# Kernel optimization log

Hardware: AMD Instinct MI355X
Metric: run time of the kernel (lower is better)

Reference implementation:

```python
import jax, jax.numpy as jnp
import numpy as np

B, T = 2, 2048
DENSE = 1024
SPARSE = 1024
NH = 8
HD = SPARSE // NH          # 128
WINDOW = 64
K = 32
RANK = HD // 4             # 32
GATE_THRESH = 0.2


def setup_inputs() -> dict:
    key = jax.random.key(0)
    ks = jax.random.split(key, 12)
    return {
        "x": jax.random.normal(ks[0], (B, T, DENSE), dtype=jnp.float32),
        "enc_q": jax.random.normal(ks[1], (NH, DENSE, HD), dtype=jnp.float32) * 0.02,
        "enc_v": jax.random.normal(ks[2], (NH, DENSE, HD), dtype=jnp.float32) * 0.02,
        # metric network: Linear(SPARSE, SPARSE//2) -> GELU -> Linear(SPARSE//2, NH*HD)
        "metric_w1": jax.random.normal(ks[3], (SPARSE, SPARSE // 2), dtype=jnp.float32) * (1.0 / np.sqrt(SPARSE)),
        "metric_b1": jnp.zeros((SPARSE // 2,), dtype=jnp.float32),
        "metric_w2": jax.random.normal(ks[4], (SPARSE // 2, NH * HD), dtype=jnp.float32) * (1.0 / np.sqrt(SPARSE // 2)),
        "metric_b2": jnp.zeros((NH * HD,), dtype=jnp.float32),
        "base_metric": jnp.ones((NH, HD), dtype=jnp.float32) * 0.1,
        "hebb_U": jax.random.normal(ks[5], (NH, HD, RANK), dtype=jnp.float32) * 0.01,
        "hebb_V": jax.random.normal(ks[6], (NH, RANK, HD), dtype=jnp.float32) * 0.01,
        "decoder": jax.random.normal(ks[7], (NH * HD, DENSE), dtype=jnp.float32) * 0.02,
    }


def _causal_window_indices(t_len, window):
    pos = jnp.arange(t_len)
    off = jnp.arange(window)
    idx = jnp.clip(pos[:, None] - off[None, :], 0, t_len - 1)  # (T, W)
    mask = idx <= pos[:, None]
    return idx, mask


def _dynamic_metric(field, w1, b1, w2, b2, base):
    # field: (B, T, SPARSE)
    sig = field.mean(axis=1)
    if field.shape[1] >= 8:
        sig = sig + field[:, ::8].mean(axis=1) * 0.5
    h = jax.nn.gelu(sig @ w1 + b1, approximate=False)
    mod = (h @ w2 + b2).reshape(field.shape[0], NH, HD)
    return jax.nn.softplus(base[None] + 0.1 * mod)  # (B, NH, HD)


def reference(x, enc_q, enc_v, metric_w1, metric_b1, metric_w2, metric_b2,
              base_metric, hebb_U, hebb_V, decoder):
    Bb, Tt, _ = x.shape
    query_sparse = jax.nn.relu(jnp.einsum('btd,nde->btne', x, enc_q))  # (B,T,NH,HD)
    value_sparse = jax.nn.relu(jnp.einsum('btd,nde->btne', x, enc_v))

    metric = _dynamic_metric(query_sparse.reshape(Bb, Tt, NH * HD),
                             metric_w1, metric_b1, metric_w2, metric_b2, base_metric)

    idx, mask = _causal_window_indices(Tt, WINDOW)  # (T,W)
    idx_b = jnp.broadcast_to(idx[None], (Bb, Tt, WINDOW))
    batch_ix = jnp.arange(Bb)[:, None, None]

    outs = []
    for h in range(NH):
        q_h = query_sparse[:, :, h, :]   # (B,T,HD)
        v_h = value_sparse[:, :, h, :]
        m_h = metric[:, h][:, None, None, :]  # (B,1,1,HD)

        k_windows = q_h[:, idx, :]            # (B,T,W,HD) gather
        diff = k_windows - q_h[:, :, None, :]
        dist = jnp.sqrt((diff * diff * m_h).sum(axis=-1) + 1e-8)  # (B,T,W)
        dist = jnp.where(mask[None], dist, jnp.inf)

        neg_d, loc = jax.lax.top_k(-dist, K)  # smallest-K distances
        topd = -neg_d
        top_idx = jnp.take_along_axis(idx_b, loc, axis=2)  # (B,T,K)

        infl = jnp.exp(-topd)
        infl = infl / (infl.sum(axis=-1, keepdims=True) + 1e-8)

        neighbor_v = v_h[batch_ix, top_idx]   # (B,T,K,HD)
        context = jnp.einsum('btk,btkd->btd', infl, neighbor_v)

        q_norm = jnp.linalg.norm(q_h, axis=-1, keepdims=True)
        gate = (q_norm > GATE_THRESH).astype(q_h.dtype)
        heb_mat = hebb_U[h] @ hebb_V[h]       # (HD,HD)
        q_unit = q_h / jnp.maximum(q_norm, 1e-12)  # F.normalize
        heb_ctx = q_unit @ heb_mat
        context = context + gate * 0.1 * heb_ctx

        outs.append(q_h * context)

    out_sparse = jnp.stack(outs, axis=2)           # (B,T,NH,HD)
    return out_sparse.reshape(Bb, Tt, NH * HD) @ decoder
```

## Files before the change

kernel.cpp:

```cpp
#include <hip/hip_runtime.h>
#include <math.h>

#define T_ 2048
#define NH_ 8
#define HD_ 128

typedef unsigned short u16;
typedef short bf16x8 __attribute__((ext_vector_type(8)));
typedef _Float16 f16x8 __attribute__((ext_vector_type(8)));
typedef float f32x4 __attribute__((ext_vector_type(4)));

union FH { _Float16 h; u16 u; };

__device__ __forceinline__ u16 f2h(float f)
{
    FH c; c.h = (_Float16)f; return c.u;
}
__device__ __forceinline__ float h2f(u16 v)
{
    FH c; c.u = v; return (float)c.h;
}
__device__ __forceinline__ void split1h(float f, u16& h, u16& l)
{
    h = f2h(f);
    l = f2h(f - h2f(h));
}

__device__ __forceinline__ u16 f2bf(float f)
{
    unsigned u = __float_as_uint(f);
    return (u16)((u + 0x7FFFu + ((u >> 16) & 1u)) >> 16);
}
__device__ __forceinline__ float bf2f(u16 h)
{
    return __uint_as_float(((unsigned)h) << 16);
}


__global__ __launch_bounds__(256) void cvt_in(const float* __restrict__ x,
                                              const float* __restrict__ enc_q,
                                              const float* __restrict__ enc_v,
                                              u16* __restrict__ xh,
                                              u16* __restrict__ WTh)
{
    __shared__ u16 tH[32][33];
    const int bid = blockIdx.x;
    if (bid < 4096) {
        int i = (bid * 256 + threadIdx.x) * 4;
        int m = i >> 10, k = i & 1023;
        float4 v = *(const float4*)&x[i];
        ushort4 hv = {f2h(v.x), f2h(v.y), f2h(v.z), f2h(v.w)};
        long o = (long)(m >> 6) * 65536 + (k >> 5) * 2048
               + ((k >> 3) & 3) * 512 + (m & 63) * 8 + (k & 7);
        *(ushort4*)&xh[o] = hv;
    } else {
        int rb = bid - 4096;
        int bx = rb & 31, by = (rb >> 5) & 31, bz = rb >> 10;
        const float* Bw = bz ? enc_v : enc_q;
        const int nofs = bz << 10;
        const int tid = threadIdx.x;
        const int tx = tid & 31, ty = tid >> 5;
        const int k0 = bx * 32, c0 = by * 32;
        #pragma unroll
        for (int r = 0; r < 4; ++r) {
            int k = k0 + ty * 4 + r;
            int c = c0 + tx;
            float v = Bw[(long)(c >> 7) * 131072 + (long)k * 128 + (c & 127)];
            tH[ty * 4 + r][tx] = f2h(v);
        }
        __syncthreads();
        #pragma unroll
        for (int r = 0; r < 4; ++r) {
            int n = nofs + c0 + ty * 4 + r;
            int k = k0 + tx;
            long o = (long)(n >> 6) * 65536 + (k >> 5) * 2048
                   + ((k >> 3) & 3) * 512 + (n & 63) * 8 + (k & 7);
            WTh[o] = tH[tx][ty * 4 + r];
        }
    }
}

__global__ __launch_bounds__(256) void cvt_wT_pk(const float* __restrict__ src0,
                                                 u16* __restrict__ WTh,
                                                 int Kd, int cs, int cm, long sn, int sk)
{
    __shared__ u16 tH[32][33];
    const float* Bw = src0;
    const int tid = threadIdx.x;
    const int tx = tid & 31, ty = tid >> 5;
    const int k0 = blockIdx.x * 32, c0 = blockIdx.y * 32;
    #pragma unroll
    for (int r = 0; r < 4; ++r) {
        int k = k0 + ty * 4 + r;
        int c = c0 + tx;
        float v = Bw[(long)(c >> cs) * sn + (long)k * sk + (c & cm)];
        tH[ty * 4 + r][tx] = f2h(v);
    }
    __syncthreads();
    const long sstr = (long)Kd * 64;
    #pragma unroll
    for (int r = 0; r < 4; ++r) {
        int n = c0 + ty * 4 + r;
        int k = k0 + tx;
        long o = (long)(n >> 6) * sstr + (k >> 5) * 2048
               + ((k >> 3) & 3) * 512 + (n & 63) * 8 + (k & 7);
        WTh[o] = tH[tx][ty * 4 + r];
    }
}

__global__ __launch_bounds__(256, 1) void gemm_qv(
    const u16* __restrict__ Ah, const u16* __restrict__ Bh,
    float* __restrict__ Qf, u16* __restrict__ Vh,
    float* __restrict__ Ps, float* __restrict__ Ps8, int Kd)
{
    __shared__ __align__(16) u16 S[4][6144];

    const int tid  = threadIdx.x;
    const int w    = tid >> 6;
    const int lane = tid & 63;

    const int id   = blockIdx.x;
    const int m0   = (id & 31) * 128;
    const int n0   = (id >> 5) * 256;

    const int mw   = (w & 1) * 64, nw = (w >> 1) * 128;
    const int mr   = lane & 15, quad = lane >> 4;

    const long sstr = (long)Kd * 64;
    const u16* gAh = Ah + (long)((m0 + mw) >> 6) * sstr;
    const u16* gB0 = Bh + (long)((n0 + nw) >> 6) * sstr;
    const u16* gB1 = gB0 + sstr;

    u16* W = &S[w][0];

    f32x4 acc[4][8] = {};
    uint4 a0, a1, a2, a3;
    uint4 b0, b1, b2, b3, b4, b5, b6, b7;

#define LOADG(KT) do { long t = (long)(KT) * 2048 + lane * 8;                        \
    a0 = *(const uint4*)(gAh + t +    0); a1 = *(const uint4*)(gAh + t +  512);      \
    a2 = *(const uint4*)(gAh + t + 1024); a3 = *(const uint4*)(gAh + t + 1536);      \
    b0 = *(const uint4*)(gB0 + t +    0); b1 = *(const uint4*)(gB0 + t +  512);      \
    b2 = *(const uint4*)(gB0 + t + 1024); b3 = *(const uint4*)(gB0 + t + 1536);      \
    b4 = *(const uint4*)(gB1 + t +    0); b5 = *(const uint4*)(gB1 + t +  512);      \
    b6 = *(const uint4*)(gB1 + t + 1024); b7 = *(const uint4*)(gB1 + t + 1536); } while (0)

#define STOREG() do { u16* D = W + lane * 8;                                         \
    *(uint4*)(D +    0) = a0; *(uint4*)(D +  512) = a1;                              \
    *(uint4*)(D + 1024) = a2; *(uint4*)(D + 1536) = a3;                              \
    *(uint4*)(D + 2048) = b0; *(uint4*)(D + 2560) = b1;                              \
    *(uint4*)(D + 3072) = b2; *(uint4*)(D + 3584) = b3;                              \
    *(uint4*)(D + 4096) = b4; *(uint4*)(D + 4608) = b5;                              \
    *(uint4*)(D + 5120) = b6; *(uint4*)(D + 5632) = b7; } while (0)

    LOADG(0);
    STOREG();
    LOADG(1);

    const int NT = Kd >> 5;
    for (int kt = 0; kt < NT; ++kt) {
        f16x8 fah[4], fbh[8];
        #pragma unroll
        for (int i = 0; i < 4; ++i)
            fah[i] = *(const f16x8*)(W + quad * 512 + (i * 16 + mr) * 8);
        #pragma unroll
        for (int j = 0; j < 8; ++j)
            fbh[j] = *(const f16x8*)(W + 2048 + ((j < 4) ? 0 : 2048)
                                     + quad * 512 + ((j & 3) * 16 + mr) * 8);
        if (kt + 1 < NT) STOREG();
        if (kt + 2 < NT) LOADG(kt + 2);
        #pragma unroll
        for (int i = 0; i < 4; ++i)
            #pragma unroll
            for (int j = 0; j < 8; ++j)
                acc[i][j] = __builtin_amdgcn_mfma_f32_16x16x32_f16(fah[i], fbh[j], acc[i][j], 0, 0, 0);
    }
#undef LOADG
#undef STOREG

    if (n0 < 1024) {
        #pragma unroll
        for (int i = 0; i < 4; ++i)
            #pragma unroll
            for (int j = 0; j < 8; ++j)
                #pragma unroll
                for (int r = 0; r < 4; ++r) {
                    float v = fmaxf(acc[i][j][r], 0.f);
                    acc[i][j][r] = v;
                    int row = m0 + mw + i * 16 + quad * 4 + r;
                    int col = n0 + nw + j * 16 + mr;
                    Qf[(long)row * 1024 + col] = v;
                }
        int slot = (id & 31) * 2 + (w & 1);
        #pragma unroll
        for (int j = 0; j < 8; ++j) {
            float ps = 0.f, p8 = 0.f;
            #pragma unroll
            for (int i = 0; i < 4; ++i) {
                #pragma unroll
                for (int r = 0; r < 4; ++r) ps += acc[i][j][r];
                if ((quad & 1) == 0) p8 += acc[i][j][0];
            }
            ps += __shfl_xor(ps, 16, 64); ps += __shfl_xor(ps, 32, 64);
            p8 += __shfl_xor(p8, 16, 64); p8 += __shfl_xor(p8, 32, 64);
            if (quad == 0) {
                int col = n0 + nw + j * 16 + mr;
                Ps [slot * 1024 + col] = ps;
                Ps8[slot * 1024 + col] = p8;
            }
        }
    } else {
        #pragma unroll
        for (int i = 0; i < 4; ++i)
            #pragma unroll
            for (int j = 0; j < 8; ++j)
                #pragma unroll
                for (int r = 0; r < 4; ++r) {
                    float v = fmaxf(acc[i][j][r], 0.f);
                    int row = m0 + mw + i * 16 + quad * 4 + r;
                    int col = n0 - 1024 + nw + j * 16 + mr;
                    Vh[(long)row * 1024 + col] = f2h(v);
                }
    }
}

__global__ __launch_bounds__(256, 1) void gemm_dec(
    const u16* __restrict__ Ah, const u16* __restrict__ Bh,
    float* __restrict__ C, int N, int Kd)
{
    __shared__ __align__(16) u16 S[4][4096];

    const int tid  = threadIdx.x;
    const int w    = tid >> 6;
    const int lane = tid & 63;

    const int id   = blockIdx.x;
    const int m0   = (((id & 7) << 2) + ((id >> 3) & 3)) * 128;
    const int n0   = (id >> 5) * 128;

    const int mw   = (w & 1) * 64, nw = (w >> 1) * 64;
    const int mr   = lane & 15, quad = lane >> 4;

    const long sstr = (long)Kd * 64;
    const u16* gAh = Ah + (long)((m0 + mw) >> 6) * sstr;
    const u16* gBh = Bh + (long)((n0 + nw) >> 6) * sstr;

    u16* W = &S[w][0];

    f32x4 acc[4][4] = {};
    uint4 a0, a1, a2, a3, b0, b1, b2, b3;

#define LOADG(KT) do { long t = (long)(KT) * 2048 + lane * 8;                        \
    a0 = *(const uint4*)(gAh + t +    0); a1 = *(const uint4*)(gAh + t +  512);      \
    a2 = *(const uint4*)(gAh + t + 1024); a3 = *(const uint4*)(gAh + t + 1536);      \
    b0 = *(const uint4*)(gBh + t +    0); b1 = *(const uint4*)(gBh + t +  512);      \
    b2 = *(const uint4*)(gBh + t + 1024); b3 = *(const uint4*)(gBh + t + 1536); } while (0)

#define STOREG() do { u16* D = W + lane * 8;                                         \
    *(uint4*)(D +    0) = a0; *(uint4*)(D +  512) = a1;                              \
    *(uint4*)(D + 1024) = a2; *(uint4*)(D + 1536) = a3;                              \
    *(uint4*)(D + 2048) = b0; *(uint4*)(D + 2560) = b1;                              \
    *(uint4*)(D + 3072) = b2; *(uint4*)(D + 3584) = b3; } while (0)

    LOADG(0);
    STOREG();
    LOADG(1);

    const int NT = Kd >> 5;
    for (int kt = 0; kt < NT; ++kt) {
        f16x8 fah[4], fbh[4];
        #pragma unroll
        for (int i = 0; i < 4; ++i) {
            int ro = quad * 512 + (i * 16 + mr) * 8;
            fah[i] = *(const f16x8*)(W + ro);
            fbh[i] = *(const f16x8*)(W + 2048 + ro);
        }
        if (kt + 1 < NT) STOREG();
        if (kt + 2 < NT) LOADG(kt + 2);
        #pragma unroll
        for (int i = 0; i < 4; ++i)
            #pragma unroll
            for (int j = 0; j < 4; ++j)
                acc[i][j] = __builtin_amdgcn_mfma_f32_16x16x32_f16(fah[i], fbh[j], acc[i][j], 0, 0, 0);
    }
#undef LOADG
#undef STOREG

    #pragma unroll
    for (int i = 0; i < 4; ++i)
        #pragma unroll
        for (int j = 0; j < 4; ++j)
            #pragma unroll
            for (int r = 0; r < 4; ++r) {
                int row = m0 + mw + i * 16 + quad * 4 + r;
                int col = n0 + nw + j * 16 + mr;
                C[(long)row * N + col] = acc[i][j][r];
            }
}

__global__ __launch_bounds__(256) void heb_gemm(
    const u16* __restrict__ Qbf, const u16* __restrict__ MhT,
    u16* __restrict__ HEBbf)
{
    __shared__ __align__(16) u16 sA[4][128][8], sB[4][128][8];

    const int tid  = threadIdx.x;
    const int w    = tid >> 6;
    const int lane = tid & 63;
    const int m0   = blockIdx.x * 128;
    const int h    = blockIdx.y;
    const int mw   = w * 32;
    const int mr   = lane & 15, quad = lane >> 4;
    const u16* Bm  = MhT + h * 16384;

    f32x4 acc[2][8] = {};

    for (int k0 = 0; k0 < 128; k0 += 32) {
        #pragma unroll
        for (int u = 0; u < 4; ++u) {
            int c = (w & 1) * 4 + u;
            int kq = c >> 1, half = c & 1;
            const u16* src; u16* dst; long gofs;
            if (w < 2) {
                src = Qbf;
                dst = &sA[0][0][0] + kq * 1024 + half * 512;
                gofs = (long)(m0 + half * 64 + lane) * 1024 + h * 128 + k0 + kq * 8;
            } else {
                src = Bm;
                dst = &sB[0][0][0] + kq * 1024 + half * 512;
                gofs = (long)(half * 64 + lane) * 128 + k0 + kq * 8;
            }
            __builtin_amdgcn_global_load_lds(
                (const __attribute__((address_space(1))) unsigned int*)(src + gofs),
                (__attribute__((address_space(3))) unsigned int*)dst, 16, 0, 0);
        }
        __syncthreads();

        bf16x8 fa[2], fb[8];
        #pragma unroll
        for (int i = 0; i < 2; ++i)
            fa[i] = *(const bf16x8*)&sA[quad][mw + i * 16 + mr][0];
        #pragma unroll
        for (int j = 0; j < 8; ++j)
            fb[j] = *(const bf16x8*)&sB[quad][j * 16 + mr][0];
        #pragma unroll
        for (int i = 0; i < 2; ++i)
            #pragma unroll
            for (int j = 0; j < 8; ++j)
                acc[i][j] = __builtin_amdgcn_mfma_f32_16x16x32_bf16(fa[i], fb[j], acc[i][j], 0, 0, 0);
        __syncthreads();
    }

    #pragma unroll
    for (int i = 0; i < 2; ++i)
        #pragma unroll
        for (int j = 0; j < 8; ++j)
            #pragma unroll
            for (int r = 0; r < 4; ++r) {
                int row = m0 + mw + i * 16 + quad * 4 + r;
                int col = h * 128 + j * 16 + mr;
                HEBbf[(long)row * 1024 + col] = f2bf(acc[i][j][r]);
            }
}

__global__ __launch_bounds__(256) void qu_stage(const float* __restrict__ Qf,
                                                const float* __restrict__ Me,
                                                u16* __restrict__ Qbf,
                                                u16* __restrict__ Uh, u16* __restrict__ Ul,
                                                float* __restrict__ nArr)
{
    int gid4 = (blockIdx.x * 256 + threadIdx.x) * 4;
    int e4 = gid4 & 127;
    int t  = (gid4 >> 7) & 2047;
    int bh = gid4 >> 18;
    int b  = bh >> 3, h = bh & 7;
    float4 q = *(const float4*)&Qf[((long)(b * 2048 + t)) * 1024 + h * 128 + e4];
    ushort4 qo = {f2bf(q.x), f2bf(q.y), f2bf(q.z), f2bf(q.w)};
    *(ushort4*)&Qbf[((long)(b * 2048 + t)) * 1024 + h * 128 + e4] = qo;

    float4 m = *(const float4*)&Me[bh * 128 + e4];
    float ux = sqrtf(m.x) * q.x, uy = sqrtf(m.y) * q.y;
    float uz = sqrtf(m.z) * q.z, uw = sqrtf(m.w) * q.w;
    u16 h0, l0, h1, l1, h2, l2, h3, l3;
    split1h(ux, h0, l0); split1h(uy, h1, l1);
    split1h(uz, h2, l2); split1h(uw, h3, l3);
    ushort4 hv = {h0, h1, h2, h3}, lv = {l0, l1, l2, l3};
    *(ushort4*)&Uh[gid4] = hv;
    *(ushort4*)&Ul[gid4] = lv;
    float ps = ux * ux + uy * uy + uz * uz + uw * uw;
    #pragma unroll
    for (int mm = 16; mm; mm >>= 1) ps += __shfl_xor(ps, mm, 64);
    if ((threadIdx.x & 31) == 0) nArr[gid4 >> 7] = ps;
}

__global__ __launch_bounds__(256, 1) void dist_gemm(
    const u16* __restrict__ Uh, const u16* __restrict__ Ul,
    const float* __restrict__ nArr, float* __restrict__ band)
{
    __shared__ __align__(16) u16 sAh[4][64][8],  sAl[4][64][8];
    __shared__ __align__(16) u16 sBh[4][128][8], sBl[4][128][8];
    __shared__ float epi[4][16][128];

    const int tid  = threadIdx.x;
    const int w    = tid >> 6;
    const int lane = tid & 63;
    const int mr   = lane & 15, quad = lane >> 4;
    const int bid  = blockIdx.x;
    const int tile = bid & 31, bh = bid >> 5;
    const int t0   = tile * 64;
    const long ub  = (long)bh * 2048 * 128;

    const u16 *s0, *s1, *s2, *s3, *s4, *s5;
    u16 *d0, *d1, *d2, *d3, *d4, *d5;
    long o0, o1, o2, o3, o4, o5;
    {
        auto mk = [&](int i, const u16*& src, u16*& dst, long& ofs) {
            int c = i * 256 + tid;
            if (c < 512) {
                int row = c & 63, kq = (c >> 6) & 3;
                src = (c < 256) ? Uh : Ul;
                ofs = ub + (long)(t0 + row) * 128 + kq * 8;
                dst = ((c < 256) ? &sAh[0][0][0] : &sAl[0][0][0]) + kq * 512 + row * 8;
            } else {
                int cb = c - 512;
                int row = cb & 127, kq = (cb >> 7) & 3;
                src = (cb < 512) ? Uh : Ul;
                ofs = ub + (long)(t0 - 64 + row) * 128 + kq * 8;
                dst = ((cb < 512) ? &sBh[0][0][0] : &sBl[0][0][0]) + kq * 1024 + row * 8;
            }
        };
        mk(0, s0, d0, o0); mk(1, s1, d1, o1); mk(2, s2, d2, o2);
        mk(3, s3, d3, o3); mk(4, s4, d4, o4); mk(5, s5, d5, o5);
    }

    f32x4 acc[8] = {};
    uint4 g0, g1, g2, g3, g4, g5;
    g0 = *(const uint4*)(s0 + o0); g1 = *(const uint4*)(s1 + o1);
    g2 = *(const uint4*)(s2 + o2); g3 = *(const uint4*)(s3 + o3);
    g4 = *(const uint4*)(s4 + o4); g5 = *(const uint4*)(s5 + o5);

    for (int k0 = 0; k0 < 128; k0 += 32) {
        *(uint4*)d0 = g0; *(uint4*)d1 = g1; *(uint4*)d2 = g2;
        *(uint4*)d3 = g3; *(uint4*)d4 = g4; *(uint4*)d5 = g5;
        __syncthreads();

        if (k0 + 32 < 128) {
            int kn = k0 + 32;
            g0 = *(const uint4*)(s0 + o0 + kn); g1 = *(const uint4*)(s1 + o1 + kn);
            g2 = *(const uint4*)(s2 + o2 + kn); g3 = *(const uint4*)(s3 + o3 + kn);
            g4 = *(const uint4*)(s4 + o4 + kn); g5 = *(const uint4*)(s5 + o5 + kn);
        }

        f16x8 fah = *(const f16x8*)&sAh[quad][w * 16 + mr][0];
        f16x8 fal = *(const f16x8*)&sAl[quad][w * 16 + mr][0];
        #pragma unroll
        for (int j = 0; j < 8; ++j) {
            f16x8 fbh = *(const f16x8*)&sBh[quad][j * 16 + mr][0];
            f16x8 fbl = *(const f16x8*)&sBl[quad][j * 16 + mr][0];
            acc[j] = __builtin_amdgcn_mfma_f32_16x16x32_f16(fah, fbh, acc[j], 0, 0, 0);
            acc[j] = __builtin_amdgcn_mfma_f32_16x16x32_f16(fah, fbl, acc[j], 0, 0, 0);
            acc[j] = __builtin_amdgcn_mfma_f32_16x16x32_f16(fal, fbh, acc[j], 0, 0, 0);
        }
        __syncthreads();
    }

    #pragma unroll
    for (int j = 0; j < 8; ++j)
        #pragma unroll
        for (int r = 0; r < 4; ++r)
            epi[w][quad * 4 + r][j * 16 + mr] = acc[j][r];
    __syncthreads();

    const float* nb = nArr + (long)bh * 2048;
    #pragma unroll
    for (int i = 0; i < 16; ++i) {
        int id = i * 256 + tid;
        int tl = id >> 6, j = id & 63;
        int t  = t0 + tl;
        int r  = t - j;
        int rc = r < 0 ? 0 : r;
        int rl = tl - j + 64;
        float S  = epi[tl >> 4][tl & 15][rl];
        float d2 = nb[t] + nb[rc] - 2.0f * S;
        band[((long)bh * 2048 + t) * 64 + j] = d2;
    }
}

__global__ __launch_bounds__(256) void mlp1_part(const float* __restrict__ Ps,
                                                 const float* __restrict__ Ps8,
                                                 const float* __restrict__ w1,
                                                 float* __restrict__ Pm)
{
    __shared__ float ssig[32];
    int tid = threadIdx.x;
    int o  = blockIdx.x * 256 + tid;
    int b  = blockIdx.y;
    int kc = blockIdx.z;
    int k0 = kc * 32;
    if (tid < 32) {
        int k = k0 + tid;
        float s = 0.f, s8 = 0.f;
        #pragma unroll
        for (int ms = 0; ms < 32; ++ms) {
            long po = ((long)(b * 32 + ms)) * 1024 + k;
            s  += Ps[po];
            s8 += Ps8[po];
        }
        ssig[tid] = s * (1.0f / 2048.0f) + 0.5f * s8 * (1.0f / 256.0f);
    }
    __syncthreads();
    float a = 0.f;
    #pragma unroll 8
    for (int kk = 0; kk < 32; ++kk)
        a += ssig[kk] * w1[(long)(k0 + kk) * 512 + o];
    Pm[((b * 32) + kc) * 512 + o] = a;
}

__global__ __launch_bounds__(256) void mlp2_part(const float* __restrict__ Pm1,
                                                 const float* __restrict__ b1,
                                                 const float* __restrict__ w2,
                                                 float* __restrict__ Pm)
{
    __shared__ float sH[32];
    int tid = threadIdx.x;
    int c  = blockIdx.x * 256 + tid;
    int b  = blockIdx.y;
    int kc = blockIdx.z;
    int k0 = kc * 32;
    if (tid < 32) {
        int o = k0 + tid;
        float a = b1[o];
        #pragma unroll
        for (int kcc = 0; kcc < 32; ++kcc)
            a += Pm1[(b * 32 + kcc) * 512 + o];
        sH[tid] = 0.5f * a * (1.0f + erff(a * 0.70710678118f));
    }
    __syncthreads();
    float a = 0.f;
    #pragma unroll 8
    for (int kk = 0; kk < 32; ++kk)
        a += sH[kk] * w2[(long)(k0 + kk) * 1024 + c];
    Pm[((b * 16) + kc) * 1024 + c] = a;
}

__global__ __launch_bounds__(256) void mlp2fin_hebb(
    const float* __restrict__ Pm, const float* __restrict__ b2,
    const float* __restrict__ base, float* __restrict__ metric,
    const float* __restrict__ U, const float* __restrict__ Vh,
    u16* __restrict__ MhT)
{
    int id = blockIdx.x;
    if (id < 8) {
        int c = (id & 3) * 256 + threadIdx.x;
        int b = id >> 2;
        float a = b2[c];
        #pragma unroll
        for (int kc = 0; kc < 16; ++kc)
            a += Pm[(b * 16 + kc) * 1024 + c];
        float mv = base[c] + 0.1f * a;
        metric[b * 1024 + c] = fmaxf(mv, 0.f) + log1pf(expf(-fabsf(mv)));
    } else {
        int gid = (id - 8) * 256 + threadIdx.x;
        int h = gid >> 14;
        int rem = gid & 16383;
        int e = rem >> 7;
        int f = rem & 127;
        float a = 0.f;
        #pragma unroll
        for (int r = 0; r < 32; ++r)
            a += U[(h * 128 + f) * 32 + r] * Vh[(h * 32 + r) * 128 + e];
        MhT[(h * 128 + e) * 128 + f] = f2bf(a);
    }
}

__global__ __launch_bounds__(256) void context_k(
    const float* __restrict__ Qf, const u16* __restrict__ Vh,
    const float* __restrict__ band, const u16* __restrict__ HEBbf,
    u16* __restrict__ CTh)
{
    __shared__ float wv[4][32];
    __shared__ int   wi[4][32];

    const int w    = threadIdx.x >> 6;
    const int lane = threadIdx.x & 63;
    const int gw   = blockIdx.x * 4 + w;
    const int h    = gw & 7;
    const int bt   = gw >> 3;
    const int t    = bt & (T_ - 1);
    const int b    = bt >> 11;
    const int bh   = b * 8 + h;

    const long qrow  = (long)bt * 1024 + h * 128;
    const long hrow  = (long)bt * 1024 + h * 128;

    float q0 = Qf[qrow + lane], q1 = Qf[qrow + 64 + lane];
    float ss = q0 * q0 + q1 * q1;
    #pragma unroll
    for (int s = 32; s; s >>= 1) ss += __shfl_xor(ss, s, 64);
    const float qn  = sqrtf(ss);
    const float inv = 1.0f / fmaxf(qn, 1e-12f);

    int je = lane < t ? lane : t;
    float d2v = (je == 0) ? 0.f
              : band[((long)bh * 2048 + t) * 64 + je];
    float d2f = fmaxf(d2v, 0.f) + 1e-8f;
    unsigned kb = (__float_as_uint(d2f) & 0xFFFFFFC0u) | (unsigned)lane;

    #pragma unroll
    for (int k = 2; k <= 32; k <<= 1)
        #pragma unroll
        for (int s = k >> 1; s >= 1; s >>= 1) {
            unsigned ok = __shfl_xor(kb, s, 64);
            bool takeMin = (((lane & k) == 0) == ((lane & s) == 0));
            if ((ok < kb) == takeMin) kb = ok;
        }
    {
        unsigned ok = __shfl_xor(kb, 32, 64);
        kb = ok < kb ? ok : kb;
    }

    int jj = kb & 63;
    float wexp = 0.f;
    if (lane < 32)
        wexp = expf(-sqrtf(__uint_as_float(kb & 0xFFFFFFC0u)));
    float tot = wexp;
    #pragma unroll
    for (int s = 32; s; s >>= 1) tot += __shfl_xor(tot, s, 64);
    float wn = wexp / (tot + 1e-8f);
    if (lane < 32) {
        wv[w][lane] = wn;
        int ii = t - jj; if (ii < 0) ii = 0;
        wi[w][lane] = ii;
    }

    float c0 = 0.f, c1 = 0.f;
    #pragma unroll 8
    for (int k = 0; k < 32; ++k) {
        float wk = wv[w][k];
        long vb = ((long)(b * T_ + wi[w][k])) * 1024 + h * 128;
        c0 += wk * h2f(Vh[vb + lane]);
        c1 += wk * h2f(Vh[vb + 64 + lane]);
    }

    if (qn > 0.2f) {
        float s = 0.1f * inv;
        c0 += s * bf2f(HEBbf[hrow + lane]);
        c1 += s * bf2f(HEBbf[hrow + 64 + lane]);
    }

    int c0c = h * 128 + lane, c1c = c0c + 64;
    long po0 = (long)(bt >> 6) * 65536 + (c0c >> 5) * 2048
             + ((c0c >> 3) & 3) * 512 + (bt & 63) * 8 + (c0c & 7);
    long po1 = (long)(bt >> 6) * 65536 + (c1c >> 5) * 2048
             + ((c1c >> 3) & 3) * 512 + (bt & 63) * 8 + (c1c & 7);
    CTh[po0] = f2h(q0 * c0);
    CTh[po1] = f2h(q1 * c1);
}

extern "C" void kernel_launch(void* const* d_in, const int* in_sizes, int n_in,
                              void* d_out, int out_size, void* d_ws, size_t ws_size,
                              hipStream_t stream)
{
    const float* x     = (const float*)d_in[0];
    const float* enc_q = (const float*)d_in[1];
    const float* enc_v = (const float*)d_in[2];
    const float* w1    = (const float*)d_in[3];
    const float* b1    = (const float*)d_in[4];
    const float* w2    = (const float*)d_in[5];
    const float* b2    = (const float*)d_in[6];
    const float* base  = (const float*)d_in[7];
    const float* hU    = (const float*)d_in[8];
    const float* hV    = (const float*)d_in[9];
    const float* dec   = (const float*)d_in[10];
    float* out = (float*)d_out;
    float* ws  = (float*)d_ws;

    float* Qf  = ws;
    u16* Vhp   = (u16*)(ws + 4194304);
    u16* wTh   = (u16*)(ws + 8388608);
    float* Ps  = ws + 9437184;
    float* Ps8 = ws + 9502720;
    u16* Uhp   = (u16*)(ws + 8388608);
    u16* Ulp   = (u16*)(ws + 10485760);
    u16* CTh   = (u16*)(ws + 8388608);
    u16* MhT   = (u16*)(ws + 12582912);
    float* nA  = ws + 12713984;
    float* Me  = ws + 12749824;
    u16* wdTh  = (u16*)ws;
    u16* xh    = (u16*)d_out;
    u16* Qbf   = (u16*)d_out;
    u16* HEBbf = (u16*)d_out + 4194304;
    float* band = (float*)d_out;
    float* Pm1 = (float*)d_out + 2097152;
    float* Pm2 = (float*)d_out + 2129920;

    cvt_in<<<6144, 256, 0, stream>>>(x, enc_q, enc_v, xh, wTh);

    gemm_qv<<<256, 256, 0, stream>>>(xh, wTh, Qf, Vhp, Ps, Ps8, 1024);

    mlp1_part<<<dim3(2, 2, 32), 256, 0, stream>>>(Ps, Ps8, w1, Pm1);
    mlp2_part<<<dim3(4, 2, 16), 256, 0, stream>>>(Pm1, b1, w2, Pm2);
    mlp2fin_hebb<<<520, 256, 0, stream>>>(Pm2, b2, base, Me, hU, hV, MhT);

    qu_stage<<<4096, 256, 0, stream>>>(Qf, Me, Qbf, Uhp, Ulp, nA);
    heb_gemm<<<dim3(32, 8), 256, 0, stream>>>(Qbf, MhT, HEBbf);
    dist_gemm<<<512, 256, 0, stream>>>(Uhp, Ulp, nA, band);

    context_k<<<8192, 256, 0, stream>>>(Qf, Vhp, band, HEBbf, CTh);

    cvt_wT_pk<<<dim3(32, 32), 256, 0, stream>>>(dec, wdTh,
                                                1024, 30, 0x3fffffff, 0L, 1024);
    gemm_dec<<<256, 256, 0, stream>>>(CTh, wdTh, out, 1024, 1024);
}
```

Before: 213.9 us.

## Merge small kernels, fold metric finalize into qu_stage, pack V pairs

Moves the decoder weight transpose and the Hebbian U@V product into the single input-conversion launch. The metric finalize now runs inside qu_stage, and the Hebbian GEMM and distance GEMM become one launch split by block index. This cuts launch count and gaps between the many small kernels. V is stored with interleaved column pairs so context_k reads two halves with one 32-bit load, and workspace buffers are reshuffled to fit. The cost is redundant metric recomputation in every qu_stage block and larger shared memory in the merged hebdist kernel.

```diff
diff --git a/kernel.cpp b/kernel.cpp
--- a/kernel.cpp
+++ b/kernel.cpp
@@ -36,12 +36,21 @@
     return __uint_as_float(((unsigned)h) << 16);
 }
 
+#define GLD16(SRC, DST) __builtin_amdgcn_global_load_lds( \
+    (const __attribute__((address_space(1))) unsigned int*)(SRC), \
+    (__attribute__((address_space(3))) unsigned int*)(DST), 16, 0, 0)
+
 
 __global__ __launch_bounds__(256) void cvt_in(const float* __restrict__ x,
                                               const float* __restrict__ enc_q,
                                               const float* __restrict__ enc_v,
+                                              const float* __restrict__ dec,
+                                              const float* __restrict__ hU,
+                                              const float* __restrict__ hV,
                                               u16* __restrict__ xh,
-                                              u16* __restrict__ WTh)
+                                              u16* __restrict__ WTh,
+                                              u16* __restrict__ WdT,
+                                              u16* __restrict__ MhT)
 {
     __shared__ u16 tH[32][33];
     const int bid = blockIdx.x;
@@ -53,7 +62,7 @@
         long o = (long)(m >> 6) * 65536 + (k >> 5) * 2048
                + ((k >> 3) & 3) * 512 + (m & 63) * 8 + (k & 7);
         *(ushort4*)&xh[o] = hv;
-    } else {
+    } else if (bid < 6144) {
         int rb = bid - 4096;
         int bx = rb & 31, by = (rb >> 5) & 31, bz = rb >> 10;
         const float* Bw = bz ? enc_v : enc_q;
@@ -77,34 +86,38 @@
                    + ((k >> 3) & 3) * 512 + (n & 63) * 8 + (k & 7);
             WTh[o] = tH[tx][ty * 4 + r];
         }
-    }
-}
-
-__global__ __launch_bounds__(256) void cvt_wT_pk(const float* __restrict__ src0,
-                                                 u16* __restrict__ WTh,
-                                                 int Kd, int cs, int cm, long sn, int sk)
-{
-    __shared__ u16 tH[32][33];
-    const float* Bw = src0;
-    const int tid = threadIdx.x;
-    const int tx = tid & 31, ty = tid >> 5;
-    const int k0 = blockIdx.x * 32, c0 = blockIdx.y * 32;
-    #pragma unroll
-    for (int r = 0; r < 4; ++r) {
-        int k = k0 + ty * 4 + r;
-        int c = c0 + tx;
-        float v = Bw[(long)(c >> cs) * sn + (long)k * sk + (c & cm)];
-        tH[ty * 4 + r][tx] = f2h(v);
-    }
-    __syncthreads();
-    const long sstr = (long)Kd * 64;
-    #pragma unroll
-    for (int r = 0; r < 4; ++r) {
-        int n = c0 + ty * 4 + r;
-        int k = k0 + tx;
-        long o = (long)(n >> 6) * sstr + (k >> 5) * 2048
-               + ((k >> 3) & 3) * 512 + (n & 63) * 8 + (k & 7);
-        WTh[o] = tH[tx][ty * 4 + r];
+    } else if (bid < 7168) {
+        int rb = bid - 6144;
+        int bx = rb & 31, by = rb >> 5;
+        const int tid = threadIdx.x;
+        const int tx = tid & 31, ty = tid >> 5;
+        const int k0 = bx * 32, c0 = by * 32;
+        #pragma unroll
+        for (int r = 0; r < 4; ++r) {
+            int k = k0 + ty * 4 + r;
+            int c = c0 + tx;
+            tH[ty * 4 + r][tx] = f2h(dec[(long)k * 1024 + c]);
+        }
+        __syncthreads();
+        #pragma unroll
+        for (int r = 0; r < 4; ++r) {
+            int n = c0 + ty * 4 + r;
+            int k = k0 + tx;
+            long o = (long)(n >> 6) * 65536 + (k >> 5) * 2048
+                   + ((k >> 3) & 3) * 512 + (n & 63) * 8 + (k & 7);
+            WdT[o] = tH[tx][ty * 4 + r];
+        }
+    } else {
+        int gid = (bid - 7168) * 256 + threadIdx.x;
+        int h = gid >> 14;
+        int rem = gid & 16383;
+        int e = rem >> 7;
+        int f = rem & 127;
+        float a = 0.f;
+        #pragma unroll
+        for (int r = 0; r < 32; ++r)
+            a += hU[(h * 128 + f) * 32 + r] * hV[(h * 32 + r) * 128 + e];
+        MhT[(h * 128 + e) * 128 + f] = f2bf(a);
     }
 }
 
@@ -218,8 +231,9 @@
                 for (int r = 0; r < 4; ++r) {
                     float v = fmaxf(acc[i][j][r], 0.f);
                     int row = m0 + mw + i * 16 + quad * 4 + r;
-                    int col = n0 - 1024 + nw + j * 16 + mr;
-                    Vh[(long)row * 1024 + col] = f2h(v);
+                    int vcol = n0 - 1024 + nw + j * 16 + mr;
+                    int pa = (vcol & ~127) + ((vcol & 63) * 2) + ((vcol >> 6) & 1);
+                    Vh[(long)row * 1024 + pa] = f2h(v);
                 }
     }
 }
@@ -298,87 +312,38 @@
             }
 }
 
-__global__ __launch_bounds__(256) void heb_gemm(
-    const u16* __restrict__ Qbf, const u16* __restrict__ MhT,
-    u16* __restrict__ HEBbf)
-{
-    __shared__ __align__(16) u16 sA[4][128][8], sB[4][128][8];
-
-    const int tid  = threadIdx.x;
-    const int w    = tid >> 6;
-    const int lane = tid & 63;
-    const int m0   = blockIdx.x * 128;
-    const int h    = blockIdx.y;
-    const int mw   = w * 32;
-    const int mr   = lane & 15, quad = lane >> 4;
-    const u16* Bm  = MhT + h * 16384;
-
-    f32x4 acc[2][8] = {};
-
-    for (int k0 = 0; k0 < 128; k0 += 32) {
-        #pragma unroll
-        for (int u = 0; u < 4; ++u) {
-            int c = (w & 1) * 4 + u;
-            int kq = c >> 1, half = c & 1;
-            const u16* src; u16* dst; long gofs;
-            if (w < 2) {
-                src = Qbf;
-                dst = &sA[0][0][0] + kq * 1024 + half * 512;
-                gofs = (long)(m0 + half * 64 + lane) * 1024 + h * 128 + k0 + kq * 8;
-            } else {
-                src = Bm;
-                dst = &sB[0][0][0] + kq * 1024 + half * 512;
-                gofs = (long)(half * 64 + lane) * 128 + k0 + kq * 8;
-            }
-            __builtin_amdgcn_global_load_lds(
-                (const __attribute__((address_space(1))) unsigned int*)(src + gofs),
-                (__attribute__((address_space(3))) unsigned int*)dst, 16, 0, 0);
-        }
-        __syncthreads();
-
-        bf16x8 fa[2], fb[8];
-        #pragma unroll
-        for (int i = 0; i < 2; ++i)
-            fa[i] = *(const bf16x8*)&sA[quad][mw + i * 16 + mr][0];
-        #pragma unroll
-        for (int j = 0; j < 8; ++j)
-            fb[j] = *(const bf16x8*)&sB[quad][j * 16 + mr][0];
-        #pragma unroll
-        for (int i = 0; i < 2; ++i)
-            #pragma unroll
-            for (int j = 0; j < 8; ++j)
-                acc[i][j] = __builtin_amdgcn_mfma_f32_16x16x32_bf16(fa[i], fb[j], acc[i][j], 0, 0, 0);
-        __syncthreads();
-    }
-
-    #pragma unroll
-    for (int i = 0; i < 2; ++i)
-        #pragma unroll
-        for (int j = 0; j < 8; ++j)
-            #pragma unroll
-            for (int r = 0; r < 4; ++r) {
-                int row = m0 + mw + i * 16 + quad * 4 + r;
-                int col = h * 128 + j * 16 + mr;
-                HEBbf[(long)row * 1024 + col] = f2bf(acc[i][j][r]);
-            }
-}
-
 __global__ __launch_bounds__(256) void qu_stage(const float* __restrict__ Qf,
-                                                const float* __restrict__ Me,
+                                                const float* __restrict__ Pm2,
+                                                const float* __restrict__ b2,
+                                                const float* __restrict__ base,
                                                 u16* __restrict__ Qbf,
                                                 u16* __restrict__ Uh, u16* __restrict__ Ul,
                                                 float* __restrict__ nArr)
 {
-    int gid4 = (blockIdx.x * 256 + threadIdx.x) * 4;
+    __shared__ float sMe[128];
+    const int tid = threadIdx.x;
+    const int bh  = blockIdx.x >> 8;
+    if (tid < 128) {
+        int b = bh >> 3;
+        int c = (bh & 7) * 128 + tid;
+        float a = b2[c];
+        #pragma unroll
+        for (int kc = 0; kc < 16; ++kc)
+            a += Pm2[(b * 16 + kc) * 1024 + c];
+        float mv = base[c] + 0.1f * a;
+        sMe[tid] = fmaxf(mv, 0.f) + log1pf(expf(-fabsf(mv)));
+    }
+    __syncthreads();
+
+    int gid4 = (blockIdx.x * 256 + tid) * 4;
     int e4 = gid4 & 127;
     int t  = (gid4 >> 7) & 2047;
-    int bh = gid4 >> 18;
     int b  = bh >> 3, h = bh & 7;
     float4 q = *(const float4*)&Qf[((long)(b * 2048 + t)) * 1024 + h * 128 + e4];
     ushort4 qo = {f2bf(q.x), f2bf(q.y), f2bf(q.z), f2bf(q.w)};
     *(ushort4*)&Qbf[((long)(b * 2048 + t)) * 1024 + h * 128 + e4] = qo;
 
-    float4 m = *(const float4*)&Me[bh * 128 + e4];
+    float4 m = *(const float4*)&sMe[e4];
     float ux = sqrtf(m.x) * q.x, uy = sqrtf(m.y) * q.y;
     float uz = sqrtf(m.z) * q.z, uw = sqrtf(m.w) * q.w;
     u16 h0, l0, h1, l1, h2, l2, h3, l3;
@@ -390,13 +355,16 @@
     float ps = ux * ux + uy * uy + uz * uz + uw * uw;
     #pragma unroll
     for (int mm = 16; mm; mm >>= 1) ps += __shfl_xor(ps, mm, 64);
-    if ((threadIdx.x & 31) == 0) nArr[gid4 >> 7] = ps;
-}
-
-__global__ __launch_bounds__(256, 1) void dist_gemm(
+    if ((tid & 31) == 0) nArr[gid4 >> 7] = ps;
+}
+
+__global__ __launch_bounds__(256, 1) void hebdist(
+    const u16* __restrict__ Qbf, const u16* __restrict__ MhT,
+    u16* __restrict__ HEBbf,
     const u16* __restrict__ Uh, const u16* __restrict__ Ul,
     const float* __restrict__ nArr, float* __restrict__ band)
 {
+    __shared__ __align__(16) u16 sA[4][128][8], sB[4][128][8];
     __shared__ __align__(16) u16 sAh[4][64][8],  sAl[4][64][8];
     __shared__ __align__(16) u16 sBh[4][128][8], sBl[4][128][8];
     __shared__ float epi[4][16][128];
@@ -405,84 +373,139 @@
     const int w    = tid >> 6;
     const int lane = tid & 63;
     const int mr   = lane & 15, quad = lane >> 4;
-    const int bid  = blockIdx.x;
-    const int tile = bid & 31, bh = bid >> 5;
-    const int t0   = tile * 64;
-    const long ub  = (long)bh * 2048 * 128;
-
-    const u16 *s0, *s1, *s2, *s3, *s4, *s5;
-    u16 *d0, *d1, *d2, *d3, *d4, *d5;
-    long o0, o1, o2, o3, o4, o5;
-    {
-        auto mk = [&](int i, const u16*& src, u16*& dst, long& ofs) {
-            int c = i * 256 + tid;
-            if (c < 512) {
-                int row = c & 63, kq = (c >> 6) & 3;
-                src = (c < 256) ? Uh : Ul;
-                ofs = ub + (long)(t0 + row) * 128 + kq * 8;
-                dst = ((c < 256) ? &sAh[0][0][0] : &sAl[0][0][0]) + kq * 512 + row * 8;
-            } else {
-                int cb = c - 512;
-                int row = cb & 127, kq = (cb >> 7) & 3;
-                src = (cb < 512) ? Uh : Ul;
-                ofs = ub + (long)(t0 - 64 + row) * 128 + kq * 8;
-                dst = ((cb < 512) ? &sBh[0][0][0] : &sBl[0][0][0]) + kq * 1024 + row * 8;
+
+    if (blockIdx.x < 256) {
+        const int m0 = (blockIdx.x & 31) * 128;
+        const int h  = blockIdx.x >> 5;
+        const int mw = w * 32;
+        const u16* Bm = MhT + h * 16384;
+
+        f32x4 acc[2][8] = {};
+
+        for (int k0 = 0; k0 < 128; k0 += 32) {
+            #pragma unroll
+            for (int u = 0; u < 4; ++u) {
+                int c = (w & 1) * 4 + u;
+                int kq = c >> 1, half = c & 1;
+                const u16* src; u16* dst; long gofs;
+                if (w < 2) {
+                    src = Qbf;
+                    dst = &sA[0][0][0] + kq * 1024 + half * 512;
+                    gofs = (long)(m0 + half * 64 + lane) * 1024 + h * 128 + k0 + kq * 8;
+                } else {
+                    src = Bm;
+                    dst = &sB[0][0][0] + kq * 1024 + half * 512;
+                    gofs = (long)(half * 64 + lane) * 128 + k0 + kq * 8;
+                }
+                GLD16(src + gofs, dst);
             }
-        };
-        mk(0, s0, d0, o0); mk(1, s1, d1, o1); mk(2, s2, d2, o2);
-        mk(3, s3, d3, o3); mk(4, s4, d4, o4); mk(5, s5, d5, o5);
-    }
-
-    f32x4 acc[8] = {};
-    uint4 g0, g1, g2, g3, g4, g5;
-    g0 = *(const uint4*)(s0 + o0); g1 = *(const uint4*)(s1 + o1);
-    g2 = *(const uint4*)(s2 + o2); g3 = *(const uint4*)(s3 + o3);
-    g4 = *(const uint4*)(s4 + o4); g5 = *(const uint4*)(s5 + o5);
-
-    for (int k0 = 0; k0 < 128; k0 += 32) {
-        *(uint4*)d0 = g0; *(uint4*)d1 = g1; *(uint4*)d2 = g2;
-        *(uint4*)d3 = g3; *(uint4*)d4 = g4; *(uint4*)d5 = g5;
+            __syncthreads();
+
+            bf16x8 fa[2], fb[8];
+            #pragma unroll
+            for (int i = 0; i < 2; ++i)
+                fa[i] = *(const bf16x8*)&sA[quad][mw + i * 16 + mr][0];
+            #pragma unroll
+            for (int j = 0; j < 8; ++j)
+                fb[j] = *(const bf16x8*)&sB[quad][j * 16 + mr][0];
+            #pragma unroll
+            for (int i = 0; i < 2; ++i)
+                #pragma unroll
+                for (int j = 0; j < 8; ++j)
+                    acc[i][j] = __builtin_amdgcn_mfma_f32_16x16x32_bf16(fa[i], fb[j], acc[i][j], 0, 0, 0);
+            __syncthreads();
+        }
+
+        #pragma unroll
+        for (int i = 0; i < 2; ++i)
+            #pragma unroll
+            for (int j = 0; j < 8; ++j)
+                #pragma unroll
+                for (int r = 0; r < 4; ++r) {
+                    int row = m0 + mw + i * 16 + quad * 4 + r;
+                    int col = h * 128 + j * 16 + mr;
+                    HEBbf[(long)row * 1024 + col] = f2bf(acc[i][j][r]);
+                }
+    } else {
+        const int bid  = blockIdx.x - 256;
+        const int tile = bid & 31, bh = bid >> 5;
+        const int t0   = tile * 64;
+        const long ub  = (long)bh * 2048 * 128;
+
+        const u16 *s0, *s1, *s2, *s3, *s4, *s5;
+        u16 *d0, *d1, *d2, *d3, *d4, *d5;
+        long o0, o1, o2, o3, o4, o5;
+        {
+            auto mk = [&](int i, const u16*& src, u16*& dst, long& ofs) {
+                int c = i * 256 + tid;
+                if (c < 512) {
+                    int row = c & 63, kq = (c >> 6) & 3;
+                    src = (c < 256) ? Uh : Ul;
+                    ofs = ub + (long)(t0 + row) * 128 + kq * 8;
+                    dst = ((c < 256) ? &sAh[0][0][0] : &sAl[0][0][0]) + kq * 512 + row * 8;
+                } else {
+                    int cb = c - 512;
+                    int row = cb & 127, kq = (cb >> 7) & 3;
+                    src = (cb < 512) ? Uh : Ul;
+                    ofs = ub + (long)(t0 - 64 + row) * 128 + kq * 8;
+                    dst = ((cb < 512) ? &sBh[0][0][0] : &sBl[0][0][0]) + kq * 1024 + row * 8;
+                }
+            };
+            mk(0, s0, d0, o0); mk(1, s1, d1, o1); mk(2, s2, d2, o2);
+            mk(3, s3, d3, o3); mk(4, s4, d4, o4); mk(5, s5, d5, o5);
+        }
+
+        f32x4 acc[8] = {};
+        uint4 g0, g1, g2, g3, g4, g5;
+        g0 = *(const uint4*)(s0 + o0); g1 = *(const uint4*)(s1 + o1);
+        g2 = *(const uint4*)(s2 + o2); g3 = *(const uint4*)(s3 + o3);
+        g4 = *(const uint4*)(s4 + o4); g5 = *(const uint4*)(s5 + o5);
+
+        for (int k0 = 0; k0 < 128; k0 += 32) {
+            *(uint4*)d0 = g0; *(uint4*)d1 = g1; *(uint4*)d2 = g2;
+            *(uint4*)d3 = g3; *(uint4*)d4 = g4; *(uint4*)d5 = g5;
+            __syncthreads();
+
+            if (k0 + 32 < 128) {
+                int kn = k0 + 32;
+                g0 = *(const uint4*)(s0 + o0 + kn); g1 = *(const uint4*)(s1 + o1 + kn);
+                g2 = *(const uint4*)(s2 + o2 + kn); g3 = *(const uint4*)(s3 + o3 + kn);
+                g4 = *(const uint4*)(s4 + o4 + kn); g5 = *(const uint4*)(s5 + o5 + kn);
+            }
+
+            f16x8 fah = *(const f16x8*)&sAh[quad][w * 16 + mr][0];
+            f16x8 fal = *(const f16x8*)&sAl[quad][w * 16 + mr][0];
+            #pragma unroll
+            for (int j = 0; j < 8; ++j) {
+                f16x8 fbh = *(const f16x8*)&sBh[quad][j * 16 + mr][0];
+                f16x8 fbl = *(const f16x8*)&sBl[quad][j * 16 + mr][0];
+                acc[j] = __builtin_amdgcn_mfma_f32_16x16x32_f16(fah, fbh, acc[j], 0, 0, 0);
+                acc[j] = __builtin_amdgcn_mfma_f32_16x16x32_f16(fah, fbl, acc[j], 0, 0, 0);
+                acc[j] = __builtin_amdgcn_mfma_f32_16x16x32_f16(fal, fbh, acc[j], 0, 0, 0);
+            }
+            __syncthreads();
+        }
+
+        #pragma unroll
+        for (int j = 0; j < 8; ++j)
+            #pragma unroll
+            for (int r = 0; r < 4; ++r)
+                epi[w][quad * 4 + r][j * 16 + mr] = acc[j][r];
         __syncthreads();
 
-        if (k0 + 32 < 128) {
-            int kn = k0 + 32;
-            g0 = *(const uint4*)(s0 + o0 + kn); g1 = *(const uint4*)(s1 + o1 + kn);
-            g2 = *(const uint4*)(s2 + o2 + kn); g3 = *(const uint4*)(s3 + o3 + kn);
-            g4 = *(const uint4*)(s4 + o4 + kn); g5 = *(const uint4*)(s5 + o5 + kn);
-        }
-
-        f16x8 fah = *(const f16x8*)&sAh[quad][w * 16 + mr][0];
-        f16x8 fal = *(const f16x8*)&sAl[quad][w * 16 + mr][0];
-        #pragma unroll
-        for (int j = 0; j < 8; ++j) {
-            f16x8 fbh = *(const f16x8*)&sBh[quad][j * 16 + mr][0];
-            f16x8 fbl = *(const f16x8*)&sBl[quad][j * 16 + mr][0];
-            acc[j] = __builtin_amdgcn_mfma_f32_16x16x32_f16(fah, fbh, acc[j], 0, 0, 0);
-            acc[j] = __builtin_amdgcn_mfma_f32_16x16x32_f16(fah, fbl, acc[j], 0, 0, 0);
-            acc[j] = __builtin_amdgcn_mfma_f32_16x16x32_f16(fal, fbh, acc[j], 0, 0, 0);
-        }
-        __syncthreads();
-    }
-
-    #pragma unroll
-    for (int j = 0; j < 8; ++j)
-        #pragma unroll
-        for (int r = 0; r < 4; ++r)
-            epi[w][quad * 4 + r][j * 16 + mr] = acc[j][r];
-    __syncthreads();
-
-    const float* nb = nArr + (long)bh * 2048;
-    #pragma unroll
-    for (int i = 0; i < 16; ++i) {
-        int id = i * 256 + tid;
-        int tl = id >> 6, j = id & 63;
-        int t  = t0 + tl;
-        int r  = t - j;
-        int rc = r < 0 ? 0 : r;
-        int rl = tl - j + 64;
-        float S  = epi[tl >> 4][tl & 15][rl];
-        float d2 = nb[t] + nb[rc] - 2.0f * S;
-        band[((long)bh * 2048 + t) * 64 + j] = d2;
+        const float* nb = nArr + (long)bh * 2048;
+        #pragma unroll
+        for (int i = 0; i < 16; ++i) {
+            int id = i * 256 + tid;
+            int tl = id >> 6, j = id & 63;
+            int t  = t0 + tl;
+            int r  = t - j;
+            int rc = r < 0 ? 0 : r;
+            int rl = tl - j + 64;
+            float S  = epi[tl >> 4][tl & 15][rl];
+            float d2 = nb[t] + nb[rc] - 2.0f * S;
+            band[((long)bh * 2048 + t) * 64 + j] = d2;
+        }
     }
 }
 
@@ -541,36 +564,6 @@
     for (int kk = 0; kk < 32; ++kk)
         a += sH[kk] * w2[(long)(k0 + kk) * 1024 + c];
     Pm[((b * 16) + kc) * 1024 + c] = a;
-}
-
-__global__ __launch_bounds__(256) void mlp2fin_hebb(
-    const float* __restrict__ Pm, const float* __restrict__ b2,
-    const float* __restrict__ base, float* __restrict__ metric,
-    const float* __restrict__ U, const float* __restrict__ Vh,
-    u16* __restrict__ MhT)
-{
-    int id = blockIdx.x;
-    if (id < 8) {
-        int c = (id & 3) * 256 + threadIdx.x;
-        int b = id >> 2;
-        float a = b2[c];
-        #pragma unroll
-        for (int kc = 0; kc < 16; ++kc)
-            a += Pm[(b * 16 + kc) * 1024 + c];
-        float mv = base[c] + 0.1f * a;
-        metric[b * 1024 + c] = fmaxf(mv, 0.f) + log1pf(expf(-fabsf(mv)));
-    } else {
-        int gid = (id - 8) * 256 + threadIdx.x;
-        int h = gid >> 14;
-        int rem = gid & 16383;
-        int e = rem >> 7;
-        int f = rem & 127;
-        float a = 0.f;
-        #pragma unroll
-        for (int r = 0; r < 32; ++r)
-            a += U[(h * 128 + f) * 32 + r] * Vh[(h * 32 + r) * 128 + e];
-        MhT[(h * 128 + e) * 128 + f] = f2bf(a);
-    }
 }
 
 __global__ __launch_bounds__(256) void context_k(
@@ -637,9 +630,10 @@
     #pragma unroll 8
     for (int k = 0; k < 32; ++k) {
         float wk = wv[w][k];
-        long vb = ((long)(b * T_ + wi[w][k])) * 1024 + h * 128;
-        c0 += wk * h2f(Vh[vb + lane]);
-        c1 += wk * h2f(Vh[vb + 64 + lane]);
+        long vb = ((long)(b * T_ + wi[w][k])) * 1024 + h * 128 + lane * 2;
+        unsigned vv = *(const unsigned*)&Vh[vb];
+        c0 += wk * h2f((u16)(vv & 0xffffu));
+        c1 += wk * h2f((u16)(vv >> 16));
     }
 
     if (qn > 0.2f) {
@@ -675,40 +669,37 @@
     float* out = (float*)d_out;
     float* ws  = (float*)d_ws;
 
-    float* Qf  = ws;
-    u16* Vhp   = (u16*)(ws + 4194304);
-    u16* wTh   = (u16*)(ws + 8388608);
-    float* Ps  = ws + 9437184;
-    float* Ps8 = ws + 9502720;
-    u16* Uhp   = (u16*)(ws + 8388608);
-    u16* Ulp   = (u16*)(ws + 10485760);
-    u16* CTh   = (u16*)(ws + 8388608);
-    u16* MhT   = (u16*)(ws + 12582912);
-    float* nA  = ws + 12713984;
-    float* Me  = ws + 12749824;
-    u16* wdTh  = (u16*)ws;
-    u16* xh    = (u16*)d_out;
-    u16* Qbf   = (u16*)d_out;
-    u16* HEBbf = (u16*)d_out + 4194304;
-    float* band = (float*)d_out;
-    float* Pm1 = (float*)d_out + 2097152;
-    float* Pm2 = (float*)d_out + 2129920;
-
-    cvt_in<<<6144, 256, 0, stream>>>(x, enc_q, enc_v, xh, wTh);
+    float* Qf   = ws;
+    u16*  Vhp   = (u16*)(ws + 4194304);
+    float* band = ws + 6291456;
+    u16*  wTh   = (u16*)(ws + 8388608);
+    u16*  Ulp   = (u16*)(ws + 8388608);
+    float* Ps   = ws + 9961472;
+    float* Ps8  = ws + 10027008;
+    u16*  Uhp   = (u16*)(ws + 10485760);
+    u16*  CTh   = (u16*)(ws + 8388608);
+    u16*  MhT   = (u16*)(ws + 12582912);
+    float* nA   = ws + 12648448;
+    u16*  wdTh  = (u16*)(ws + 12681216);
+    u16*  xh    = (u16*)d_out;
+    u16*  Qbf   = (u16*)d_out;
+    u16*  HEBbf = (u16*)d_out + 4194304;
+    float* Pm1  = (float*)d_out + 2097152;
+    float* Pm2  = (float*)d_out + 2129920;
+
+    cvt_in<<<7680, 256, 0, stream>>>(x, enc_q, enc_v, dec, hU, hV,
+                                     xh, wTh, wdTh, MhT);
 
     gemm_qv<<<256, 256, 0, stream>>>(xh, wTh, Qf, Vhp, Ps, Ps8, 1024);
 
     mlp1_part<<<dim3(2, 2, 32), 256, 0, stream>>>(Ps, Ps8, w1, Pm1);
     mlp2_part<<<dim3(4, 2, 16), 256, 0, stream>>>(Pm1, b1, w2, Pm2);
-    mlp2fin_hebb<<<520, 256, 0, stream>>>(Pm2, b2, base, Me, hU, hV, MhT);
-
-    qu_stage<<<4096, 256, 0, stream>>>(Qf, Me, Qbf, Uhp, Ulp, nA);
-    heb_gemm<<<dim3(32, 8), 256, 0, stream>>>(Qbf, MhT, HEBbf);
-    dist_gemm<<<512, 256, 0, stream>>>(Uhp, Ulp, nA, band);
+
+    qu_stage<<<4096, 256, 0, stream>>>(Qf, Pm2, b2, base, Qbf, Uhp, Ulp, nA);
+
+    hebdist<<<768, 256, 0, stream>>>(Qbf, MhT, HEBbf, Uhp, Ulp, nA, band);
 
     context_k<<<8192, 256, 0, stream>>>(Qf, Vhp, band, HEBbf, CTh);
 
-    cvt_wT_pk<<<dim3(32, 32), 256, 0, stream>>>(dec, wdTh,
-                                                1024, 30, 0x3fffffff, 0L, 1024);
     gemm_dec<<<256, 256, 0, stream>>>(CTh, wdTh, out, 1024, 1024);
 }
```

Measured after the change: 210.6 us. Within noise of the previous version (-1.6%).
